# Kernel tuning notes

Measured on AMD Instinct MI355X. Metric: run time of the kernel, lower is better.

Reference implementation:

```python
import jax, jax.numpy as jnp
import numpy as np


def setup_inputs() -> dict:
    key = jax.random.key(0)
    kq, kk, kv, kl = jax.random.split(key, 4)
    B, Nq, Nk, D, Dv = 16, 2048, 2048, 128, 128
    queries = jax.random.normal(kq, (B, Nq, D), dtype=jnp.float32)
    keys = jax.random.normal(kk, (B, Nk, D), dtype=jnp.float32)
    values = jax.random.normal(kv, (B, Nk, Dv), dtype=jnp.float32)
    valid_lens = jax.random.randint(kl, (B,), 0, 2048, dtype=jnp.int64)
    return {"queries": queries, "keys": keys, "values": values, "valid_lens": valid_lens}


def reference(queries, keys, values, valid_lens):
    # queries: (B, Nq, d), keys: (B, Nk, d), values: (B, Nk, dv), valid_lens: (B,)
    d = queries.shape[-1]
    scores = jnp.einsum('bqd,bkd->bqk', queries, keys) / jnp.sqrt(jnp.asarray(d, queries.dtype))
    # masked_softmax: original sets masked score positions to 1e-8 (NOT -inf) before softmax
    nk = scores.shape[-1]
    mask = jnp.arange(nk)[None, :] < valid_lens[:, None]  # (B, Nk)
    scores = jnp.where(mask[:, None, :], scores, jnp.asarray(1e-8, scores.dtype))
    attn = jax.nn.softmax(scores, axis=-1)
    # dropout rate 0.0 -> identity (eval semantics)
    return jnp.einsum('bqk,bkv->bqv', attn, values)
```

## Files before the change

kernel.cpp:

```cpp
#include <hip/hip_runtime.h>
#include <stdint.h>

#define BATCH 16
#define NQ    2048
#define NK    2048
#define DD    128
#define DVV   128

typedef __bf16 bf16_t;
typedef __bf16 bf16x2 __attribute__((ext_vector_type(2)));
typedef __bf16 bf16x4 __attribute__((ext_vector_type(4)));
typedef __bf16 bf16x8 __attribute__((ext_vector_type(8)));
typedef float  f32x4  __attribute__((ext_vector_type(4)));

#define QB_OFF  ((size_t)0)
#define KB_OFF  ((size_t)8 * 1024 * 1024)
#define VT_OFF  ((size_t)16 * 1024 * 1024)
#define SUF_OFF ((size_t)24 * 1024 * 1024)
#define OP_OFF  (SUF_OFF + 65536)
#define LP_OFF  (OP_OFF + (size_t)1024 * 8192 * 4)
#define WS_NEED (LP_OFF + (size_t)1024 * 64 * 4)

__device__ __forceinline__ int load_valid_len(const int* VL, int b) {
  bool looks64 = true;
#pragma unroll
  for (int i = 0; i < 16; ++i) {
    int hi = VL[2 * i + 1];
    unsigned lo = (unsigned)VL[2 * i];
    looks64 = looks64 && (hi == 0) && (lo <= 2048u);
  }
  int L = looks64 ? VL[2 * b] : VL[b];
  return min(max(L, 0), NK);
}

__device__ __forceinline__ void gld16(const void* g, void* l) {
  __builtin_amdgcn_global_load_lds(
      (const __attribute__((address_space(1))) unsigned int*)g,
      (__attribute__((address_space(3))) unsigned int*)l, 16, 0, 0);
}

__device__ __forceinline__ f32x4 mfma16(bf16x8 a, bf16x8 b, f32x4 c) {
  return __builtin_amdgcn_mfma_f32_16x16x32_bf16(a, b, c, 0, 0, 0);
}

__global__ void prep_kernel(const float* __restrict__ Q, const float* __restrict__ K,
                            const float* __restrict__ V, const int* __restrict__ VL,
                            bf16_t* __restrict__ Qb, bf16_t* __restrict__ Kb,
                            bf16_t* __restrict__ Vt, float* __restrict__ sufV) {
  __shared__ bf16_t tile[128 * 72];
  const int bid = blockIdx.x;
  const int t = threadIdx.x;
  if (bid < 1024) {
    const float sc = 0.1275174307f;
    size_t base = ((size_t)bid * 256 + t) * 32;
    const size_t NQK = (size_t)BATCH * NQ * DD;
    bool isQ = base < NQK;
    const float* src = isQ ? (Q + base) : (K + (base - NQK));
    bf16_t* dst = isQ ? (Qb + base) : (Kb + (base - NQK));
    float s = isQ ? sc : 1.0f;
#pragma unroll
    for (int i = 0; i < 4; ++i) {
      float4 a = ((const float4*)src)[i * 2];
      float4 b = ((const float4*)src)[i * 2 + 1];
      bf16x8 o;
      o[0] = (bf16_t)(a.x * s); o[1] = (bf16_t)(a.y * s);
      o[2] = (bf16_t)(a.z * s); o[3] = (bf16_t)(a.w * s);
      o[4] = (bf16_t)(b.x * s); o[5] = (bf16_t)(b.y * s);
      o[6] = (bf16_t)(b.z * s); o[7] = (bf16_t)(b.w * s);
      ((bf16x8*)dst)[i] = o;
    }
    return;
  }
  int v = bid - 1024;
  int b = v & 15, kt = v >> 4;
  int L = load_valid_len(VL, b);
  int m = t & 31;
  int g = t >> 5;
  int r2 = m * 2;
  int k0g = kt * 64 + r2;
  const float* src = V + ((size_t)b * NK + k0g) * DVV;
  float sacc[4][4];
#pragma unroll
  for (int i = 0; i < 4; ++i)
#pragma unroll
    for (int j = 0; j < 4; ++j) sacc[i][j] = 0.f;
  bool a0 = (k0g >= L), a1 = (k0g + 1 >= L);
#pragma unroll
  for (int i = 0; i < 4; ++i) {
    int d4 = g * 4 + i * 32;
    float4 u0 = *(const float4*)(src + d4);
    float4 u1 = *(const float4*)(src + DVV + d4);
    *(bf16x2*)&tile[(d4 + 0) * 72 + r2] = (bf16x2){(bf16_t)u0.x, (bf16_t)u1.x};
    *(bf16x2*)&tile[(d4 + 1) * 72 + r2] = (bf16x2){(bf16_t)u0.y, (bf16_t)u1.y};
    *(bf16x2*)&tile[(d4 + 2) * 72 + r2] = (bf16x2){(bf16_t)u0.z, (bf16_t)u1.z};
    *(bf16x2*)&tile[(d4 + 3) * 72 + r2] = (bf16x2){(bf16_t)u0.w, (bf16_t)u1.w};
    if (a0) { sacc[i][0] += u0.x; sacc[i][1] += u0.y; sacc[i][2] += u0.z; sacc[i][3] += u0.w; }
    if (a1) { sacc[i][0] += u1.x; sacc[i][1] += u1.y; sacc[i][2] += u1.z; sacc[i][3] += u1.w; }
  }
  __syncthreads();
#pragma unroll
  for (int off = 1; off < 32; off <<= 1)
#pragma unroll
    for (int i = 0; i < 4; ++i)
#pragma unroll
      for (int j = 0; j < 4; ++j) sacc[i][j] += __shfl_xor(sacc[i][j], off, 64);
  if (m == 0) {
#pragma unroll
    for (int i = 0; i < 4; ++i)
#pragma unroll
      for (int j = 0; j < 4; ++j)
        atomicAdd(&sufV[b * 128 + g * 4 + i * 32 + j], sacc[i][j]);
  }
  int dv = t >> 1, half = t & 1;
  bf16_t* dst = Vt + (size_t)b * DVV * NK + (size_t)dv * NK + kt * 64 + half * 32;
  const bf16_t* srow = &tile[dv * 72 + half * 32];
#pragma unroll
  for (int j = 0; j < 4; ++j)
    *(bf16x8*)(dst + j * 8) = *(const bf16x8*)(srow + j * 8);
}

__launch_bounds__(256, 2)
__global__ void attn_kernel(const bf16_t* __restrict__ Qb, const bf16_t* __restrict__ Kb,
                            const bf16_t* __restrict__ Vt, const int* __restrict__ VL,
                            float* __restrict__ Opart, float* __restrict__ lpart) {
  __shared__ bf16_t sK[2][64 * 128];
  __shared__ bf16_t sVt[2][128 * 64];
  __shared__ bf16_t sP[4][16 * 64];

  const int flat = blockIdx.x;
  const int s  = flat & 1;
  const int b  = (flat >> 1) & 15;
  const int qt = flat >> 5;
  const int L  = load_valid_len(VL, b);
  const int ktiles = (L + 63) >> 6;
  const int t0 = (s * ktiles) >> 1;
  const int t1 = ((s + 1) * ktiles) >> 1;

  const int tid = threadIdx.x;
  const int wave = tid >> 6;
  const int lane = tid & 63;
  const int col = lane & 15;
  const int quad = lane >> 4;

  bf16x8 qf[4];
  {
    const bf16_t* qrow = Qb + ((size_t)b * NQ + qt * 64 + wave * 16 + col) * DD + quad * 8;
#pragma unroll
    for (int ks = 0; ks < 4; ++ks) qf[ks] = *(const bf16x8*)(qrow + ks * 32);
  }

  const char* Kbyte = (const char*)Kb + (size_t)b * NK * DD * 2;
  const char* Vbyte = (const char*)Vt + (size_t)b * DVV * NK * 2;
  int koff[4], voff[4];
#pragma unroll
  for (int i = 0; i < 4; ++i) {
    int krow = wave * 16 + i * 4 + (lane >> 4);
    koff[i] = krow * 256 + (((lane & 15) ^ (krow & 15)) * 16);
    int vrow = wave * 32 + i * 8 + (lane >> 3);
    voff[i] = vrow * (NK * 2) + (((lane & 7) ^ ((lane >> 3) & 7)) * 16);
  }
  bf16_t* pw = sP[wave];

  f32x4 Oacc[8];
#pragma unroll
  for (int o = 0; o < 8; ++o) Oacc[o] = (f32x4){0.f, 0.f, 0.f, 0.f};
  float lsum[4] = {0.f, 0.f, 0.f, 0.f};

  auto issueTile = [&](int kt, int bufi) {
    const char* kb = Kbyte + (size_t)kt * 16384;
    const char* vb = Vbyte + (size_t)kt * 128;
    bf16_t* kl = &sK[bufi][wave * 2048];
    bf16_t* vl = &sVt[bufi][wave * 2048];
#pragma unroll
    for (int i = 0; i < 4; ++i) {
      gld16(kb + koff[i], kl + i * 512);
      gld16(vb + voff[i], vl + i * 512);
    }
  };

  if (t0 < t1) issueTile(t0, 0);
  int bufi = 0;
  for (int kt = t0; kt < t1; ++kt) {
    if (kt + 1 < t1) {
      issueTile(kt + 1, bufi ^ 1);
      asm volatile("s_waitcnt vmcnt(8)\n\ts_barrier" ::: "memory");
    } else {
      asm volatile("s_waitcnt vmcnt(0)\n\ts_barrier" ::: "memory");
    }

    const bf16_t* kb_ = sK[bufi];
    const bf16_t* vb_ = sVt[bufi];

    f32x4 sc[4];
#pragma unroll
    for (int nt = 0; nt < 4; ++nt) sc[nt] = (f32x4){0.f, 0.f, 0.f, 0.f};
#pragma unroll
    for (int ks = 0; ks < 4; ++ks) {
      bf16x8 a = qf[ks];
#pragma unroll
      for (int nt = 0; nt < 4; ++nt) {
        bf16x8 bb = *(const bf16x8*)&kb_[(nt * 16 + col) * 128 + (((ks * 4 + quad) ^ col) * 8)];
        sc[nt] = mfma16(a, bb, sc[nt]);
      }
    }

    const int key0 = kt * 64;
#pragma unroll
    for (int nt = 0; nt < 4; ++nt) {
      bool valid = (key0 + nt * 16 + col) < L;
#pragma unroll
      for (int r = 0; r < 4; ++r) {
        float p = __builtin_amdgcn_exp2f(sc[nt][r]);
        p = valid ? p : 0.f;
        lsum[r] += p;
        int row = quad * 4 + r;
        int keyc = nt * 16 + col;
        int phys = ((keyc >> 3) ^ (row & 7));
        pw[row * 64 + phys * 8 + (keyc & 7)] = (bf16_t)p;
      }
    }

#pragma unroll
    for (int ks2 = 0; ks2 < 2; ++ks2) {
      bf16x8 a = *(const bf16x8*)&pw[col * 64 + (((ks2 * 4 + quad) ^ (col & 7)) * 8)];
#pragma unroll
      for (int o = 0; o < 8; ++o) {
        bf16x8 bb = *(const bf16x8*)&vb_[(o * 16 + col) * 64 + (((ks2 * 4 + quad) ^ (col & 7)) * 8)];
        Oacc[o] = mfma16(a, bb, Oacc[o]);
      }
    }
    asm volatile("s_barrier" ::: "memory");
    bufi ^= 1;
  }

#pragma unroll
  for (int off = 1; off < 16; off <<= 1)
#pragma unroll
    for (int r = 0; r < 4; ++r) lsum[r] += __shfl_xor(lsum[r], off, 64);

  float* Op = Opart + (size_t)flat * 8192;
#pragma unroll
  for (int o = 0; o < 8; ++o)
#pragma unroll
    for (int r = 0; r < 4; ++r)
      Op[(wave * 16 + quad * 4 + r) * 128 + o * 16 + col] = Oacc[o][r];
  if (col == 0) {
#pragma unroll
    for (int r = 0; r < 4; ++r)
      lpart[flat * 64 + wave * 16 + quad * 4 + r] = lsum[r];
  }
}

__global__ void combine_kernel(const float* __restrict__ Opart, const float* __restrict__ lpart,
                               const float* __restrict__ sufV, const int* __restrict__ VL,
                               float* __restrict__ Out) {
  int b = blockIdx.x & 15, qt = blockIdx.x >> 4;
  int L = load_valid_len(VL, b);
  int slot0 = qt * 32 + b * 2;
  int t = threadIdx.x;
  int dv = t & 127, rh = t >> 7;
  const float* O0 = Opart + (size_t)slot0 * 8192;
  const float* O1 = O0 + 8192;
  float suf = sufV[b * 128 + dv];
  float wmask = (float)(NK - L);
  float* Ob = Out + ((size_t)b * NQ + qt * 64) * DVV;
  for (int r = rh; r < 64; r += 2) {
    float l = lpart[slot0 * 64 + r] + lpart[slot0 * 64 + 64 + r] + wmask;
    Ob[(size_t)r * 128 + dv] = (O0[r * 128 + dv] + O1[r * 128 + dv] + suf) / l;
  }
}

#define KSTR 152
#define VSTR 88
#define PSTR 72

__global__ void suffix_fb(const float* __restrict__ V, const int* __restrict__ VL,
                          float* __restrict__ ws) {
  int b = blockIdx.x;
  int kc = blockIdx.y;
  int L = load_valid_len(VL, b);
  int k0 = kc * 128, k1 = k0 + 128;
  int lo = max(L, k0);
  int t = threadIdx.x;
  int dv = t & 127;
  int h = t >> 7;
  float s = 0.f;
  for (int k = lo + h; k < k1; k += 2)
    s += V[((size_t)b * NK + k) * DVV + dv];
  __shared__ float part[128];
  if (h == 0) part[dv] = s;
  __syncthreads();
  if (h == 1) atomicAdd(&ws[b * DVV + dv], part[dv] + s);
}

__launch_bounds__(256, 2)
__global__ void attn_fb(const float* __restrict__ Q, const float* __restrict__ K,
                        const float* __restrict__ V, const int* __restrict__ VL,
                        const float* __restrict__ sufV, float* __restrict__ Out) {
  const int flat = blockIdx.x;
  const int b  = flat & 15;
  const int qt = flat >> 4;
  const int L  = load_valid_len(VL, b);

  __shared__ bf16_t sK2[64 * KSTR];
  __shared__ bf16_t sVT2[128 * VSTR];
  __shared__ bf16_t sP2[4 * 16 * PSTR];

  const int tid  = threadIdx.x;
  const int wave = tid >> 6;
  const int lane = tid & 63;
  const int col  = lane & 15;
  const int quad = lane >> 4;

  const float* Qb = Q + ((size_t)b * NQ + qt * 64 + wave * 16) * DD;
  const float* Kb = K + (size_t)b * NK * DD;
  const float* Vb = V + (size_t)b * NK * DVV;

  bf16x8 qf[4];
  {
    const float scq = 0.08838834764831845f;
    const float* qrow = Qb + (size_t)col * DD + quad * 8;
#pragma unroll
    for (int ks = 0; ks < 4; ++ks) {
      float4 u0 = *(const float4*)(qrow + ks * 32);
      float4 u1 = *(const float4*)(qrow + ks * 32 + 4);
      bf16x8 f;
      f[0] = (bf16_t)(u0.x * scq); f[1] = (bf16_t)(u0.y * scq);
      f[2] = (bf16_t)(u0.z * scq); f[3] = (bf16_t)(u0.w * scq);
      f[4] = (bf16_t)(u1.x * scq); f[5] = (bf16_t)(u1.y * scq);
      f[6] = (bf16_t)(u1.z * scq); f[7] = (bf16_t)(u1.w * scq);
      qf[ks] = f;
    }
  }

  f32x4 Oacc[8];
#pragma unroll
  for (int o = 0; o < 8; ++o) Oacc[o] = (f32x4){0.f, 0.f, 0.f, 0.f};
  float m_i[4], l_i[4];
#pragma unroll
  for (int r = 0; r < 4; ++r) { m_i[r] = -1e30f; l_i[r] = 0.f; }

  const int ktiles = (L + 63) >> 6;
  for (int kt = 0; kt < ktiles; ++kt) {
    {
      int r0 = tid >> 5;
      int d4 = (tid & 31) * 4;
      const float* src = Kb + ((size_t)(kt * 64) + r0) * DD + d4;
#pragma unroll
      for (int i = 0; i < 8; ++i) {
        float4 u = *(const float4*)(src + (size_t)i * 8 * DD);
        bf16x4 w4 = {(bf16_t)u.x, (bf16_t)u.y, (bf16_t)u.z, (bf16_t)u.w};
        *(bf16x4*)&sK2[(r0 + i * 8) * KSTR + d4] = w4;
      }
    }
    {
      int r2 = (tid & 31) * 2;
      int dbase = (tid >> 5) * 4;
#pragma unroll
      for (int i = 0; i < 4; ++i) {
        int d4 = dbase + i * 32;
        const float* s0 = Vb + ((size_t)(kt * 64) + r2) * DVV + d4;
        float4 u0 = *(const float4*)s0;
        float4 u1 = *(const float4*)(s0 + DVV);
        *(bf16x2*)&sVT2[(d4 + 0) * VSTR + r2] = (bf16x2){(bf16_t)u0.x, (bf16_t)u1.x};
        *(bf16x2*)&sVT2[(d4 + 1) * VSTR + r2] = (bf16x2){(bf16_t)u0.y, (bf16_t)u1.y};
        *(bf16x2*)&sVT2[(d4 + 2) * VSTR + r2] = (bf16x2){(bf16_t)u0.z, (bf16_t)u1.z};
        *(bf16x2*)&sVT2[(d4 + 3) * VSTR + r2] = (bf16x2){(bf16_t)u0.w, (bf16_t)u1.w};
      }
    }
    __syncthreads();

    f32x4 sv4[4];
#pragma unroll
    for (int nt = 0; nt < 4; ++nt) sv4[nt] = (f32x4){0.f, 0.f, 0.f, 0.f};
#pragma unroll
    for (int ks = 0; ks < 4; ++ks) {
      bf16x8 a = qf[ks];
#pragma unroll
      for (int nt = 0; nt < 4; ++nt) {
        bf16x8 bb = *(const bf16x8*)&sK2[(nt * 16 + col) * KSTR + ks * 32 + quad * 8];
        sv4[nt] = mfma16(a, bb, sv4[nt]);
      }
    }

    const int key0 = kt * 64;
    float sv[4][4];
    float mloc[4] = {-1e30f, -1e30f, -1e30f, -1e30f};
#pragma unroll
    for (int nt = 0; nt < 4; ++nt) {
      int key = key0 + nt * 16 + col;
      bool valid = key < L;
#pragma unroll
      for (int r = 0; r < 4; ++r) {
        float v = valid ? sv4[nt][r] : -1e30f;
        sv[nt][r] = v;
        mloc[r] = fmaxf(mloc[r], v);
      }
    }
#pragma unroll
    for (int off = 1; off < 16; off <<= 1)
#pragma unroll
      for (int r = 0; r < 4; ++r) mloc[r] = fmaxf(mloc[r], __shfl_xor(mloc[r], off, 64));
    float al[4];
#pragma unroll
    for (int r = 0; r < 4; ++r) {
      float mn = fmaxf(m_i[r], mloc[r]);
      al[r] = __expf(m_i[r] - mn);
      m_i[r] = mn;
    }
    float lloc[4] = {0.f, 0.f, 0.f, 0.f};
#pragma unroll
    for (int nt = 0; nt < 4; ++nt)
#pragma unroll
      for (int r = 0; r < 4; ++r) {
        float p = __expf(sv[nt][r] - m_i[r]);
        sv[nt][r] = p;
        lloc[r] += p;
      }
#pragma unroll
    for (int off = 1; off < 16; off <<= 1)
#pragma unroll
      for (int r = 0; r < 4; ++r) lloc[r] += __shfl_xor(lloc[r], off, 64);
#pragma unroll
    for (int r = 0; r < 4; ++r) l_i[r] = l_i[r] * al[r] + lloc[r];
#pragma unroll
    for (int o = 0; o < 8; ++o)
#pragma unroll
      for (int r = 0; r < 4; ++r) Oacc[o][r] *= al[r];

    bf16_t* pw = &sP2[wave * 16 * PSTR];
#pragma unroll
    for (int nt = 0; nt < 4; ++nt)
#pragma unroll
      for (int r = 0; r < 4; ++r)
        pw[(quad * 4 + r) * PSTR + nt * 16 + col] = (bf16_t)sv[nt][r];

#pragma unroll
    for (int ks2 = 0; ks2 < 2; ++ks2) {
      bf16x8 a = *(const bf16x8*)&pw[(lane & 15) * PSTR + ks2 * 32 + quad * 8];
#pragma unroll
      for (int o = 0; o < 8; ++o) {
        bf16x8 bb = *(const bf16x8*)&sVT2[(o * 16 + col) * VSTR + ks2 * 32 + quad * 8];
        Oacc[o] = mfma16(a, bb, Oacc[o]);
      }
    }
    __syncthreads();
  }

  if (L < NK) {
    const float c = 1e-8f;
    const float w = (float)(NK - L);
    float a2[4], ec[4];
#pragma unroll
    for (int r = 0; r < 4; ++r) {
      float mn = fmaxf(m_i[r], c);
      a2[r] = __expf(m_i[r] - mn);
      ec[r] = __expf(c - mn);
      l_i[r] = l_i[r] * a2[r] + w * ec[r];
    }
    const float* sfv = sufV + b * DVV;
#pragma unroll
    for (int o = 0; o < 8; ++o) {
      float svv = sfv[o * 16 + col];
#pragma unroll
      for (int r = 0; r < 4; ++r) Oacc[o][r] = Oacc[o][r] * a2[r] + ec[r] * svv;
    }
  }

  float invl[4];
#pragma unroll
  for (int r = 0; r < 4; ++r) invl[r] = 1.0f / l_i[r];

  float* Ob = Out + ((size_t)b * NQ + qt * 64 + wave * 16) * DVV;
#pragma unroll
  for (int o = 0; o < 8; ++o)
#pragma unroll
    for (int r = 0; r < 4; ++r)
      Ob[(size_t)(quad * 4 + r) * DVV + o * 16 + col] = Oacc[o][r] * invl[r];
}

extern "C" void kernel_launch(void* const* d_in, const int* in_sizes, int n_in,
                              void* d_out, int out_size, void* d_ws, size_t ws_size,
                              hipStream_t stream) {
  const float* Q  = (const float*)d_in[0];
  const float* K  = (const float*)d_in[1];
  const float* V  = (const float*)d_in[2];
  const int*   VL = (const int*)d_in[3];
  float* out = (float*)d_out;

  if (ws_size >= WS_NEED) {
    char* ws = (char*)d_ws;
    bf16_t* Qb = (bf16_t*)(ws + QB_OFF);
    bf16_t* Kb = (bf16_t*)(ws + KB_OFF);
    bf16_t* Vt = (bf16_t*)(ws + VT_OFF);
    float* sufV = (float*)(ws + SUF_OFF);
    float* Opart = (float*)(ws + OP_OFF);
    float* lpart = (float*)(ws + LP_OFF);

    hipMemsetAsync(sufV, 0, BATCH * DVV * sizeof(float), stream);
    prep_kernel<<<1536, 256, 0, stream>>>(Q, K, V, VL, Qb, Kb, Vt, sufV);
    attn_kernel<<<BATCH * (NQ / 64) * 2, 256, 0, stream>>>(Qb, Kb, Vt, VL, Opart, lpart);
    combine_kernel<<<BATCH * (NQ / 64), 256, 0, stream>>>(Opart, lpart, sufV, VL, out);
  } else {
    float* ws = (float*)d_ws;
    hipMemsetAsync(ws, 0, BATCH * DVV * sizeof(float), stream);
    dim3 g1(BATCH, 16);
    suffix_fb<<<g1, 256, 0, stream>>>(V, VL, ws);
    attn_fb<<<BATCH * (NQ / 64), 256, 0, stream>>>(Q, K, V, VL, ws, out);
  }
}
```

Measured before the change: 164.2 us.

## Replace split-K with longest-first batch scheduling and fuse combine into attention

Drops the two-way key split and the separate combine kernel. Each attention block now handles one full query tile, and the epilogue adds the masked-value suffix sum and divides by the row sum before writing output directly. An extra prep block sorts batches by valid length and writes a snake-ordered schedule so long batches launch first and load balances across 512 blocks. This removes the Opart/lpart round trip and one launch, at the cost of less parallelism (512 vs 1024 blocks) and longer per-block serial loops.

```diff
diff --git a/kernel.cpp b/kernel.cpp
--- a/kernel.cpp
+++ b/kernel.cpp
@@ -13,13 +13,12 @@
 typedef __bf16 bf16x8 __attribute__((ext_vector_type(8)));
 typedef float  f32x4  __attribute__((ext_vector_type(4)));
 
-#define QB_OFF  ((size_t)0)
-#define KB_OFF  ((size_t)8 * 1024 * 1024)
-#define VT_OFF  ((size_t)16 * 1024 * 1024)
-#define SUF_OFF ((size_t)24 * 1024 * 1024)
-#define OP_OFF  (SUF_OFF + 65536)
-#define LP_OFF  (OP_OFF + (size_t)1024 * 8192 * 4)
-#define WS_NEED (LP_OFF + (size_t)1024 * 64 * 4)
+#define QB_OFF   ((size_t)0)
+#define KB_OFF   ((size_t)8 * 1024 * 1024)
+#define VT_OFF   ((size_t)16 * 1024 * 1024)
+#define SUF_OFF  ((size_t)24 * 1024 * 1024)
+#define SCH_OFF  (SUF_OFF + 65536)
+#define WS_NEED  (SCH_OFF + 4096)
 
 __device__ __forceinline__ int load_valid_len(const int* VL, int b) {
   bool looks64 = true;
@@ -46,8 +45,10 @@
 __global__ void prep_kernel(const float* __restrict__ Q, const float* __restrict__ K,
                             const float* __restrict__ V, const int* __restrict__ VL,
                             bf16_t* __restrict__ Qb, bf16_t* __restrict__ Kb,
-                            bf16_t* __restrict__ Vt, float* __restrict__ sufV) {
+                            bf16_t* __restrict__ Vt, float* __restrict__ sufV,
+                            int* __restrict__ sched) {
   __shared__ bf16_t tile[128 * 72];
+  __shared__ int bs[16];
   const int bid = blockIdx.x;
   const int t = threadIdx.x;
   if (bid < 1024) {
@@ -71,70 +72,88 @@
     }
     return;
   }
-  int v = bid - 1024;
-  int b = v & 15, kt = v >> 4;
-  int L = load_valid_len(VL, b);
-  int m = t & 31;
-  int g = t >> 5;
-  int r2 = m * 2;
-  int k0g = kt * 64 + r2;
-  const float* src = V + ((size_t)b * NK + k0g) * DVV;
-  float sacc[4][4];
-#pragma unroll
-  for (int i = 0; i < 4; ++i)
-#pragma unroll
-    for (int j = 0; j < 4; ++j) sacc[i][j] = 0.f;
-  bool a0 = (k0g >= L), a1 = (k0g + 1 >= L);
-#pragma unroll
-  for (int i = 0; i < 4; ++i) {
-    int d4 = g * 4 + i * 32;
-    float4 u0 = *(const float4*)(src + d4);
-    float4 u1 = *(const float4*)(src + DVV + d4);
-    *(bf16x2*)&tile[(d4 + 0) * 72 + r2] = (bf16x2){(bf16_t)u0.x, (bf16_t)u1.x};
-    *(bf16x2*)&tile[(d4 + 1) * 72 + r2] = (bf16x2){(bf16_t)u0.y, (bf16_t)u1.y};
-    *(bf16x2*)&tile[(d4 + 2) * 72 + r2] = (bf16x2){(bf16_t)u0.z, (bf16_t)u1.z};
-    *(bf16x2*)&tile[(d4 + 3) * 72 + r2] = (bf16x2){(bf16_t)u0.w, (bf16_t)u1.w};
-    if (a0) { sacc[i][0] += u0.x; sacc[i][1] += u0.y; sacc[i][2] += u0.z; sacc[i][3] += u0.w; }
-    if (a1) { sacc[i][0] += u1.x; sacc[i][1] += u1.y; sacc[i][2] += u1.z; sacc[i][3] += u1.w; }
+  if (bid < 1536) {
+    int v = bid - 1024;
+    int b = v & 15, kt = v >> 4;
+    int L = load_valid_len(VL, b);
+    int m = t & 31;
+    int g = t >> 5;
+    int r2 = m * 2;
+    int k0g = kt * 64 + r2;
+    const float* src = V + ((size_t)b * NK + k0g) * DVV;
+    float sacc[4][4];
+#pragma unroll
+    for (int i = 0; i < 4; ++i)
+#pragma unroll
+      for (int j = 0; j < 4; ++j) sacc[i][j] = 0.f;
+    bool a0 = (k0g >= L), a1 = (k0g + 1 >= L);
+#pragma unroll
+    for (int i = 0; i < 4; ++i) {
+      int d4 = g * 4 + i * 32;
+      float4 u0 = *(const float4*)(src + d4);
+      float4 u1 = *(const float4*)(src + DVV + d4);
+      *(bf16x2*)&tile[(d4 + 0) * 72 + r2] = (bf16x2){(bf16_t)u0.x, (bf16_t)u1.x};
+      *(bf16x2*)&tile[(d4 + 1) * 72 + r2] = (bf16x2){(bf16_t)u0.y, (bf16_t)u1.y};
+      *(bf16x2*)&tile[(d4 + 2) * 72 + r2] = (bf16x2){(bf16_t)u0.z, (bf16_t)u1.z};
+      *(bf16x2*)&tile[(d4 + 3) * 72 + r2] = (bf16x2){(bf16_t)u0.w, (bf16_t)u1.w};
+      if (a0) { sacc[i][0] += u0.x; sacc[i][1] += u0.y; sacc[i][2] += u0.z; sacc[i][3] += u0.w; }
+      if (a1) { sacc[i][0] += u1.x; sacc[i][1] += u1.y; sacc[i][2] += u1.z; sacc[i][3] += u1.w; }
+    }
+    __syncthreads();
+#pragma unroll
+    for (int off = 1; off < 32; off <<= 1)
+#pragma unroll
+      for (int i = 0; i < 4; ++i)
+#pragma unroll
+        for (int j = 0; j < 4; ++j) sacc[i][j] += __shfl_xor(sacc[i][j], off, 64);
+    if (m == 0) {
+#pragma unroll
+      for (int i = 0; i < 4; ++i)
+#pragma unroll
+        for (int j = 0; j < 4; ++j)
+          atomicAdd(&sufV[b * 128 + g * 4 + i * 32 + j], sacc[i][j]);
+    }
+    int dv = t >> 1, half = t & 1;
+    bf16_t* dst = Vt + (size_t)b * DVV * NK + (size_t)dv * NK + kt * 64 + half * 32;
+    const bf16_t* srow = &tile[dv * 72 + half * 32];
+#pragma unroll
+    for (int j = 0; j < 4; ++j)
+      *(bf16x8*)(dst + j * 8) = *(const bf16x8*)(srow + j * 8);
+    return;
+  }
+  if (t == 0) {
+    int Ls[16], idx[16];
+#pragma unroll
+    for (int i = 0; i < 16; ++i) { Ls[i] = load_valid_len(VL, i); idx[i] = i; }
+    for (int i = 1; i < 16; ++i) {
+      int lv = Ls[i], iv = idx[i], j = i - 1;
+      while (j >= 0 && Ls[j] < lv) { Ls[j + 1] = Ls[j]; idx[j + 1] = idx[j]; --j; }
+      Ls[j + 1] = lv; idx[j + 1] = iv;
+    }
+#pragma unroll
+    for (int i = 0; i < 16; ++i) bs[i] = idx[i];
   }
   __syncthreads();
-#pragma unroll
-  for (int off = 1; off < 32; off <<= 1)
-#pragma unroll
-    for (int i = 0; i < 4; ++i)
-#pragma unroll
-      for (int j = 0; j < 4; ++j) sacc[i][j] += __shfl_xor(sacc[i][j], off, 64);
-  if (m == 0) {
-#pragma unroll
-    for (int i = 0; i < 4; ++i)
-#pragma unroll
-      for (int j = 0; j < 4; ++j)
-        atomicAdd(&sufV[b * 128 + g * 4 + i * 32 + j], sacc[i][j]);
-  }
-  int dv = t >> 1, half = t & 1;
-  bf16_t* dst = Vt + (size_t)b * DVV * NK + (size_t)dv * NK + kt * 64 + half * 32;
-  const bf16_t* srow = &tile[dv * 72 + half * 32];
-#pragma unroll
-  for (int j = 0; j < 4; ++j)
-    *(bf16x8*)(dst + j * 8) = *(const bf16x8*)(srow + j * 8);
+  for (int j = t; j < 512; j += 256) {
+    int r = (j < 256) ? j : (767 - j);
+    sched[j] = (bs[r >> 5] << 5) | (r & 31);
+  }
 }
 
 __launch_bounds__(256, 2)
 __global__ void attn_kernel(const bf16_t* __restrict__ Qb, const bf16_t* __restrict__ Kb,
                             const bf16_t* __restrict__ Vt, const int* __restrict__ VL,
-                            float* __restrict__ Opart, float* __restrict__ lpart) {
+                            const float* __restrict__ sufV, const int* __restrict__ sched,
+                            float* __restrict__ Out) {
   __shared__ bf16_t sK[2][64 * 128];
   __shared__ bf16_t sVt[2][128 * 64];
   __shared__ bf16_t sP[4][16 * 64];
 
-  const int flat = blockIdx.x;
-  const int s  = flat & 1;
-  const int b  = (flat >> 1) & 15;
-  const int qt = flat >> 5;
+  const int unit = sched[blockIdx.x];
+  const int b  = (unit >> 5) & 15;
+  const int qt = unit & 31;
   const int L  = load_valid_len(VL, b);
   const int ktiles = (L + 63) >> 6;
-  const int t0 = (s * ktiles) >> 1;
-  const int t1 = ((s + 1) * ktiles) >> 1;
 
   const int tid = threadIdx.x;
   const int wave = tid >> 6;
@@ -178,10 +197,10 @@
     }
   };
 
-  if (t0 < t1) issueTile(t0, 0);
+  if (ktiles > 0) issueTile(0, 0);
   int bufi = 0;
-  for (int kt = t0; kt < t1; ++kt) {
-    if (kt + 1 < t1) {
+  for (int kt = 0; kt < ktiles; ++kt) {
+    if (kt + 1 < ktiles) {
       issueTile(kt + 1, bufi ^ 1);
       asm volatile("s_waitcnt vmcnt(8)\n\ts_barrier" ::: "memory");
     } else {
@@ -238,35 +257,18 @@
 #pragma unroll
     for (int r = 0; r < 4; ++r) lsum[r] += __shfl_xor(lsum[r], off, 64);
 
-  float* Op = Opart + (size_t)flat * 8192;
-#pragma unroll
-  for (int o = 0; o < 8; ++o)
+  const float wmask = (float)(NK - L);
+  float invl[4];
+#pragma unroll
+  for (int r = 0; r < 4; ++r) invl[r] = 1.0f / (lsum[r] + wmask);
+  const float* sfv = sufV + b * DVV;
+  float* Ob = Out + ((size_t)b * NQ + qt * 64 + wave * 16) * DVV;
+#pragma unroll
+  for (int o = 0; o < 8; ++o) {
+    float svv = sfv[o * 16 + col];
 #pragma unroll
     for (int r = 0; r < 4; ++r)
-      Op[(wave * 16 + quad * 4 + r) * 128 + o * 16 + col] = Oacc[o][r];
-  if (col == 0) {
-#pragma unroll
-    for (int r = 0; r < 4; ++r)
-      lpart[flat * 64 + wave * 16 + quad * 4 + r] = lsum[r];
-  }
-}
-
-__global__ void combine_kernel(const float* __restrict__ Opart, const float* __restrict__ lpart,
-                               const float* __restrict__ sufV, const int* __restrict__ VL,
-                               float* __restrict__ Out) {
-  int b = blockIdx.x & 15, qt = blockIdx.x >> 4;
-  int L = load_valid_len(VL, b);
-  int slot0 = qt * 32 + b * 2;
-  int t = threadIdx.x;
-  int dv = t & 127, rh = t >> 7;
-  const float* O0 = Opart + (size_t)slot0 * 8192;
-  const float* O1 = O0 + 8192;
-  float suf = sufV[b * 128 + dv];
-  float wmask = (float)(NK - L);
-  float* Ob = Out + ((size_t)b * NQ + qt * 64) * DVV;
-  for (int r = rh; r < 64; r += 2) {
-    float l = lpart[slot0 * 64 + r] + lpart[slot0 * 64 + 64 + r] + wmask;
-    Ob[(size_t)r * 128 + dv] = (O0[r * 128 + dv] + O1[r * 128 + dv] + suf) / l;
+      Ob[(size_t)(quad * 4 + r) * DVV + o * 16 + col] = (Oacc[o][r] + svv) * invl[r];
   }
 }
 
@@ -494,13 +496,11 @@
     bf16_t* Kb = (bf16_t*)(ws + KB_OFF);
     bf16_t* Vt = (bf16_t*)(ws + VT_OFF);
     float* sufV = (float*)(ws + SUF_OFF);
-    float* Opart = (float*)(ws + OP_OFF);
-    float* lpart = (float*)(ws + LP_OFF);
+    int* sched = (int*)(ws + SCH_OFF);
 
     hipMemsetAsync(sufV, 0, BATCH * DVV * sizeof(float), stream);
-    prep_kernel<<<1536, 256, 0, stream>>>(Q, K, V, VL, Qb, Kb, Vt, sufV);
-    attn_kernel<<<BATCH * (NQ / 64) * 2, 256, 0, stream>>>(Qb, Kb, Vt, VL, Opart, lpart);
-    combine_kernel<<<BATCH * (NQ / 64), 256, 0, stream>>>(Opart, lpart, sufV, VL, out);
+    prep_kernel<<<1537, 256, 0, stream>>>(Q, K, V, VL, Qb, Kb, Vt, sufV, sched);
+    attn_kernel<<<512, 256, 0, stream>>>(Qb, Kb, Vt, VL, sufV, sched, out);
   } else {
     float* ws = (float*)d_ws;
     hipMemsetAsync(ws, 0, BATCH * DVV * sizeof(float), stream);
```

Result: faster. 147.4 us (-10.2%).

## Double query rows per wave, fuse Q conversion, and schedule batches longest-first

Applied to the files above, without the earlier changes.

Each wave now handles 32 query rows instead of 16, so every K/V fragment read from LDS feeds two MFMAs and the K/V tile loads are amortized over 128 query rows per block. The Q fp32-to-bf16 conversion and scaling move from the prep kernel into the attention kernel, removing one workspace round-trip. Blocks are assigned to batches sorted by descending valid length, using a snake ordering to balance work across CUs. In exchange, register pressure roughly doubles for the accumulators and the grid halves to 512 blocks, which reduces parallelism.

```diff
diff --git a/kernel.cpp b/kernel.cpp
--- a/kernel.cpp
+++ b/kernel.cpp
@@ -13,13 +13,12 @@
 typedef __bf16 bf16x8 __attribute__((ext_vector_type(8)));
 typedef float  f32x4  __attribute__((ext_vector_type(4)));
 
-#define QB_OFF  ((size_t)0)
-#define KB_OFF  ((size_t)8 * 1024 * 1024)
-#define VT_OFF  ((size_t)16 * 1024 * 1024)
-#define SUF_OFF ((size_t)24 * 1024 * 1024)
-#define OP_OFF  (SUF_OFF + 65536)
-#define LP_OFF  (OP_OFF + (size_t)1024 * 8192 * 4)
-#define WS_NEED (LP_OFF + (size_t)1024 * 64 * 4)
+#define KB_OFF   ((size_t)0)
+#define VT_OFF   ((size_t)8 * 1024 * 1024)
+#define SUF_OFF  ((size_t)16 * 1024 * 1024)
+#define OP_OFF   (SUF_OFF + 65536)
+#define LP_OFF   (OP_OFF + (size_t)512 * 16384 * 4)
+#define WS_NEED  (LP_OFF + (size_t)512 * 128 * 4)
 
 __device__ __forceinline__ int load_valid_len(const int* VL, int b) {
   bool looks64 = true;
@@ -43,35 +42,29 @@
   return __builtin_amdgcn_mfma_f32_16x16x32_bf16(a, b, c, 0, 0, 0);
 }
 
-__global__ void prep_kernel(const float* __restrict__ Q, const float* __restrict__ K,
-                            const float* __restrict__ V, const int* __restrict__ VL,
-                            bf16_t* __restrict__ Qb, bf16_t* __restrict__ Kb,
-                            bf16_t* __restrict__ Vt, float* __restrict__ sufV) {
+__global__ void prep_kernel(const float* __restrict__ K, const float* __restrict__ V,
+                            const int* __restrict__ VL,
+                            bf16_t* __restrict__ Kb, bf16_t* __restrict__ Vt,
+                            float* __restrict__ sufV) {
   __shared__ bf16_t tile[128 * 72];
   const int bid = blockIdx.x;
   const int t = threadIdx.x;
-  if (bid < 1024) {
-    const float sc = 0.1275174307f;
+  if (bid < 512) {
     size_t base = ((size_t)bid * 256 + t) * 32;
-    const size_t NQK = (size_t)BATCH * NQ * DD;
-    bool isQ = base < NQK;
-    const float* src = isQ ? (Q + base) : (K + (base - NQK));
-    bf16_t* dst = isQ ? (Qb + base) : (Kb + (base - NQK));
-    float s = isQ ? sc : 1.0f;
+    const float* src = K + base;
+    bf16_t* dst = Kb + base;
 #pragma unroll
     for (int i = 0; i < 4; ++i) {
       float4 a = ((const float4*)src)[i * 2];
-      float4 b = ((const float4*)src)[i * 2 + 1];
+      float4 c = ((const float4*)src)[i * 2 + 1];
       bf16x8 o;
-      o[0] = (bf16_t)(a.x * s); o[1] = (bf16_t)(a.y * s);
-      o[2] = (bf16_t)(a.z * s); o[3] = (bf16_t)(a.w * s);
-      o[4] = (bf16_t)(b.x * s); o[5] = (bf16_t)(b.y * s);
-      o[6] = (bf16_t)(b.z * s); o[7] = (bf16_t)(b.w * s);
+      o[0] = (bf16_t)a.x; o[1] = (bf16_t)a.y; o[2] = (bf16_t)a.z; o[3] = (bf16_t)a.w;
+      o[4] = (bf16_t)c.x; o[5] = (bf16_t)c.y; o[6] = (bf16_t)c.z; o[7] = (bf16_t)c.w;
       ((bf16x8*)dst)[i] = o;
     }
     return;
   }
-  int v = bid - 1024;
+  int v = bid - 512;
   int b = v & 15, kt = v >> 4;
   int L = load_valid_len(VL, b);
   int m = t & 31;
@@ -120,33 +113,58 @@
 }
 
 __launch_bounds__(256, 2)
-__global__ void attn_kernel(const bf16_t* __restrict__ Qb, const bf16_t* __restrict__ Kb,
+__global__ void attn_kernel(const float* __restrict__ Q, const bf16_t* __restrict__ Kb,
                             const bf16_t* __restrict__ Vt, const int* __restrict__ VL,
                             float* __restrict__ Opart, float* __restrict__ lpart) {
-  __shared__ bf16_t sK[2][64 * 128];
-  __shared__ bf16_t sVt[2][128 * 64];
-  __shared__ bf16_t sP[4][16 * 64];
-
-  const int flat = blockIdx.x;
-  const int s  = flat & 1;
-  const int b  = (flat >> 1) & 15;
-  const int qt = flat >> 5;
-  const int L  = load_valid_len(VL, b);
+  __shared__ __align__(16) bf16_t sK[2][64 * 128];
+  __shared__ __align__(16) bf16_t sVt[2][128 * 64];
+  __shared__ __align__(16) bf16_t sP[4][32 * 64];
+
+  const int bid = blockIdx.x;
+  const int tid = threadIdx.x;
+
+  int Ls[16], idxs[16];
+#pragma unroll
+  for (int i = 0; i < 16; ++i) { Ls[i] = load_valid_len(VL, i); idxs[i] = i; }
+  for (int i = 1; i < 16; ++i) {
+    int lv = Ls[i], iv = idxs[i], j = i - 1;
+    while (j >= 0 && Ls[j] < lv) { Ls[j + 1] = Ls[j]; idxs[j + 1] = idxs[j]; --j; }
+    Ls[j + 1] = lv; idxs[j + 1] = iv;
+  }
+  const int r_  = (bid < 256) ? bid : (767 - bid);
+  const int b   = idxs[r_ >> 5];
+  const int L   = Ls[r_ >> 5];
+  const int sub = r_ & 31;
+  const int qt2 = sub >> 1;
+  const int s   = sub & 1;
   const int ktiles = (L + 63) >> 6;
   const int t0 = (s * ktiles) >> 1;
   const int t1 = ((s + 1) * ktiles) >> 1;
-
-  const int tid = threadIdx.x;
+  const int slot = (b * 16 + qt2) * 2 + s;
+
   const int wave = tid >> 6;
   const int lane = tid & 63;
   const int col = lane & 15;
   const int quad = lane >> 4;
 
-  bf16x8 qf[4];
+  bf16x8 qf[2][4];
   {
-    const bf16_t* qrow = Qb + ((size_t)b * NQ + qt * 64 + wave * 16 + col) * DD + quad * 8;
-#pragma unroll
-    for (int ks = 0; ks < 4; ++ks) qf[ks] = *(const bf16x8*)(qrow + ks * 32);
+    const float sc = 0.1275174307f;
+#pragma unroll
+    for (int m = 0; m < 2; ++m) {
+      const float* qrow = Q + ((size_t)b * NQ + qt2 * 128 + wave * 32 + m * 16 + col) * DD + quad * 8;
+#pragma unroll
+      for (int ks = 0; ks < 4; ++ks) {
+        float4 u0 = *(const float4*)(qrow + ks * 32);
+        float4 u1 = *(const float4*)(qrow + ks * 32 + 4);
+        bf16x8 f;
+        f[0] = (bf16_t)(u0.x * sc); f[1] = (bf16_t)(u0.y * sc);
+        f[2] = (bf16_t)(u0.z * sc); f[3] = (bf16_t)(u0.w * sc);
+        f[4] = (bf16_t)(u1.x * sc); f[5] = (bf16_t)(u1.y * sc);
+        f[6] = (bf16_t)(u1.z * sc); f[7] = (bf16_t)(u1.w * sc);
+        qf[m][ks] = f;
+      }
+    }
   }
 
   const char* Kbyte = (const char*)Kb + (size_t)b * NK * DD * 2;
@@ -161,10 +179,12 @@
   }
   bf16_t* pw = sP[wave];
 
-  f32x4 Oacc[8];
-#pragma unroll
-  for (int o = 0; o < 8; ++o) Oacc[o] = (f32x4){0.f, 0.f, 0.f, 0.f};
-  float lsum[4] = {0.f, 0.f, 0.f, 0.f};
+  f32x4 Oacc[2][8];
+#pragma unroll
+  for (int m = 0; m < 2; ++m)
+#pragma unroll
+    for (int o = 0; o < 8; ++o) Oacc[m][o] = (f32x4){0.f, 0.f, 0.f, 0.f};
+  float lsum[2][4] = {{0.f, 0.f, 0.f, 0.f}, {0.f, 0.f, 0.f, 0.f}};
 
   auto issueTile = [&](int kt, int bufi) {
     const char* kb = Kbyte + (size_t)kt * 16384;
@@ -191,16 +211,18 @@
     const bf16_t* kb_ = sK[bufi];
     const bf16_t* vb_ = sVt[bufi];
 
-    f32x4 sc[4];
-#pragma unroll
-    for (int nt = 0; nt < 4; ++nt) sc[nt] = (f32x4){0.f, 0.f, 0.f, 0.f};
+    f32x4 sc4[2][4];
+#pragma unroll
+    for (int m = 0; m < 2; ++m)
+#pragma unroll
+      for (int nt = 0; nt < 4; ++nt) sc4[m][nt] = (f32x4){0.f, 0.f, 0.f, 0.f};
 #pragma unroll
     for (int ks = 0; ks < 4; ++ks) {
-      bf16x8 a = qf[ks];
 #pragma unroll
       for (int nt = 0; nt < 4; ++nt) {
         bf16x8 bb = *(const bf16x8*)&kb_[(nt * 16 + col) * 128 + (((ks * 4 + quad) ^ col) * 8)];
-        sc[nt] = mfma16(a, bb, sc[nt]);
+        sc4[0][nt] = mfma16(qf[0][ks], bb, sc4[0][nt]);
+        sc4[1][nt] = mfma16(qf[1][ks], bb, sc4[1][nt]);
       }
     }
 
@@ -209,24 +231,29 @@
     for (int nt = 0; nt < 4; ++nt) {
       bool valid = (key0 + nt * 16 + col) < L;
 #pragma unroll
-      for (int r = 0; r < 4; ++r) {
-        float p = __builtin_amdgcn_exp2f(sc[nt][r]);
-        p = valid ? p : 0.f;
-        lsum[r] += p;
-        int row = quad * 4 + r;
-        int keyc = nt * 16 + col;
-        int phys = ((keyc >> 3) ^ (row & 7));
-        pw[row * 64 + phys * 8 + (keyc & 7)] = (bf16_t)p;
+      for (int m = 0; m < 2; ++m) {
+#pragma unroll
+        for (int r = 0; r < 4; ++r) {
+          float p = __builtin_amdgcn_exp2f(sc4[m][nt][r]);
+          p = valid ? p : 0.f;
+          lsum[m][r] += p;
+          int row = quad * 4 + r;
+          int keyc = nt * 16 + col;
+          int phys = ((keyc >> 3) ^ (row & 7));
+          pw[m * 1024 + row * 64 + phys * 8 + (keyc & 7)] = (bf16_t)p;
+        }
       }
     }
 
 #pragma unroll
     for (int ks2 = 0; ks2 < 2; ++ks2) {
-      bf16x8 a = *(const bf16x8*)&pw[col * 64 + (((ks2 * 4 + quad) ^ (col & 7)) * 8)];
+      bf16x8 a0 = *(const bf16x8*)&pw[0 * 1024 + col * 64 + (((ks2 * 4 + quad) ^ (col & 7)) * 8)];
+      bf16x8 a1 = *(const bf16x8*)&pw[1 * 1024 + col * 64 + (((ks2 * 4 + quad) ^ (col & 7)) * 8)];
 #pragma unroll
       for (int o = 0; o < 8; ++o) {
         bf16x8 bb = *(const bf16x8*)&vb_[(o * 16 + col) * 64 + (((ks2 * 4 + quad) ^ (col & 7)) * 8)];
-        Oacc[o] = mfma16(a, bb, Oacc[o]);
+        Oacc[0][o] = mfma16(a0, bb, Oacc[0][o]);
+        Oacc[1][o] = mfma16(a1, bb, Oacc[1][o]);
       }
     }
     asm volatile("s_barrier" ::: "memory");
@@ -236,36 +263,43 @@
 #pragma unroll
   for (int off = 1; off < 16; off <<= 1)
 #pragma unroll
-    for (int r = 0; r < 4; ++r) lsum[r] += __shfl_xor(lsum[r], off, 64);
-
-  float* Op = Opart + (size_t)flat * 8192;
-#pragma unroll
-  for (int o = 0; o < 8; ++o)
-#pragma unroll
-    for (int r = 0; r < 4; ++r)
-      Op[(wave * 16 + quad * 4 + r) * 128 + o * 16 + col] = Oacc[o][r];
-  if (col == 0) {
-#pragma unroll
-    for (int r = 0; r < 4; ++r)
-      lpart[flat * 64 + wave * 16 + quad * 4 + r] = lsum[r];
+    for (int m = 0; m < 2; ++m)
+#pragma unroll
+      for (int r = 0; r < 4; ++r) lsum[m][r] += __shfl_xor(lsum[m][r], off, 64);
+
+  float* Op = Opart + (size_t)slot * 16384;
+#pragma unroll
+  for (int m = 0; m < 2; ++m) {
+    int rowb = wave * 32 + m * 16 + quad * 4;
+#pragma unroll
+    for (int o = 0; o < 8; ++o)
+#pragma unroll
+      for (int r = 0; r < 4; ++r)
+        Op[(rowb + r) * 128 + o * 16 + col] = Oacc[m][o][r];
+    if (col == 0) {
+#pragma unroll
+      for (int r = 0; r < 4; ++r)
+        lpart[slot * 128 + rowb + r] = lsum[m][r];
+    }
   }
 }
 
 __global__ void combine_kernel(const float* __restrict__ Opart, const float* __restrict__ lpart,
                                const float* __restrict__ sufV, const int* __restrict__ VL,
                                float* __restrict__ Out) {
-  int b = blockIdx.x & 15, qt = blockIdx.x >> 4;
+  int u = blockIdx.x;
+  int b = u & 15, qt2 = u >> 4;
   int L = load_valid_len(VL, b);
-  int slot0 = qt * 32 + b * 2;
+  int slot0 = (b * 16 + qt2) * 2;
   int t = threadIdx.x;
   int dv = t & 127, rh = t >> 7;
-  const float* O0 = Opart + (size_t)slot0 * 8192;
-  const float* O1 = O0 + 8192;
+  const float* O0 = Opart + (size_t)slot0 * 16384;
+  const float* O1 = O0 + 16384;
   float suf = sufV[b * 128 + dv];
   float wmask = (float)(NK - L);
-  float* Ob = Out + ((size_t)b * NQ + qt * 64) * DVV;
-  for (int r = rh; r < 64; r += 2) {
-    float l = lpart[slot0 * 64 + r] + lpart[slot0 * 64 + 64 + r] + wmask;
+  float* Ob = Out + ((size_t)b * NQ + qt2 * 128) * DVV;
+  for (int r = rh; r < 128; r += 2) {
+    float l = lpart[slot0 * 128 + r] + lpart[(slot0 + 1) * 128 + r] + wmask;
     Ob[(size_t)r * 128 + dv] = (O0[r * 128 + dv] + O1[r * 128 + dv] + suf) / l;
   }
 }
@@ -490,7 +524,6 @@
 
   if (ws_size >= WS_NEED) {
     char* ws = (char*)d_ws;
-    bf16_t* Qb = (bf16_t*)(ws + QB_OFF);
     bf16_t* Kb = (bf16_t*)(ws + KB_OFF);
     bf16_t* Vt = (bf16_t*)(ws + VT_OFF);
     float* sufV = (float*)(ws + SUF_OFF);
@@ -498,9 +531,9 @@
     float* lpart = (float*)(ws + LP_OFF);
 
     hipMemsetAsync(sufV, 0, BATCH * DVV * sizeof(float), stream);
-    prep_kernel<<<1536, 256, 0, stream>>>(Q, K, V, VL, Qb, Kb, Vt, sufV);
-    attn_kernel<<<BATCH * (NQ / 64) * 2, 256, 0, stream>>>(Qb, Kb, Vt, VL, Opart, lpart);
-    combine_kernel<<<BATCH * (NQ / 64), 256, 0, stream>>>(Opart, lpart, sufV, VL, out);
+    prep_kernel<<<1024, 256, 0, stream>>>(K, V, VL, Kb, Vt, sufV);
+    attn_kernel<<<512, 256, 0, stream>>>(Q, Kb, Vt, VL, Opart, lpart);
+    combine_kernel<<<256, 256, 0, stream>>>(Opart, lpart, sufV, VL, out);
   } else {
     float* ws = (float*)d_ws;
     hipMemsetAsync(ws, 0, BATCH * DVV * sizeof(float), stream);
```

Result: no change. 162.5 us (-1.1%).
